# Kernel tuning notes

Measured on AMD Instinct MI355X. Metric: run time of the kernel, lower is better.

Reference implementation:

```python
import math
import jax, jax.numpy as jnp
import numpy as np

L, D, H, F, V, S = 4, 1024, 16, 4096, 50257, 2048
HS = D // H
EPS = 1e-5
STD = 0.02


def setup_inputs() -> dict:
    key = jax.random.key(0)
    keys = iter(jax.random.split(key, 24))

    def rn(shape):
        return (jax.random.normal(next(keys), shape, jnp.float32) * STD)

    inp = {
        "input_ids": jax.random.randint(next(keys), (1, S), 0, V, dtype=jnp.int64),
        "tok_emb": rn((V, D)),
        "pos_emb": rn((S, D)),
        # per-layer stacked params; linear weights stored [in, out]
        "Wq": rn((L, D, D)), "bq": jnp.zeros((L, D)),
        "Wk": rn((L, D, D)), "bk": jnp.zeros((L, D)),
        "Wv": rn((L, D, D)), "bv": jnp.zeros((L, D)),
        "Wo": rn((L, D, D)), "bo": jnp.zeros((L, D)),
        "W1": rn((L, D, F)), "b1": jnp.zeros((L, F)),
        "W2": rn((L, F, D)), "b2": jnp.zeros((L, D)),
        "ln1w": jnp.ones((L, D)), "ln1b": jnp.zeros((L, D)),
        "ln2w": jnp.ones((L, D)), "ln2b": jnp.zeros((L, D)),
        "lnfw": jnp.ones((D,)), "lnfb": jnp.zeros((D,)),
        "lm_head": rn((V, D)),  # torch Linear weight layout [out, in]
    }
    return inp


def _layernorm(x, w, b):
    m = jnp.mean(x, axis=-1, keepdims=True)
    v = jnp.mean(jnp.square(x - m), axis=-1, keepdims=True)
    return (x - m) * jax.lax.rsqrt(v + EPS) * w + b


def reference(input_ids, tok_emb, pos_emb, Wq, bq, Wk, bk, Wv, bv, Wo, bo,
              W1, b1, W2, b2, ln1w, ln1b, ln2w, ln2b, lnfw, lnfb, lm_head):
    B, Sq = input_ids.shape
    h = tok_emb[input_ids] + pos_emb[None, :Sq]  # [B,S,D]
    causal = jnp.tril(jnp.ones((Sq, Sq), dtype=bool))
    scale = 1.0 / math.sqrt(HS)

    def block(h, p):
        wq, bq_, wk, bk_, wv, bv_, wo, bo_, w1, b1_, w2, b2_, l1w, l1b, l2w, l2b = p
        x = _layernorm(h, l1w, l1b)
        q = (x @ wq + bq_).reshape(B, Sq, H, HS).transpose(0, 2, 1, 3)
        k = (x @ wk + bk_).reshape(B, Sq, H, HS).transpose(0, 2, 1, 3)
        v = (x @ wv + bv_).reshape(B, Sq, H, HS).transpose(0, 2, 1, 3)
        scores = jnp.einsum('bhqd,bhkd->bhqk', q, k) * scale
        scores = jnp.where(causal, scores, jnp.finfo(scores.dtype).min)
        attn = jax.nn.softmax(scores, axis=-1)  # dropout is identity at eval
        out = jnp.einsum('bhqk,bhkd->bhqd', attn, v)
        out = out.transpose(0, 2, 1, 3).reshape(B, Sq, D)
        h = h + out @ wo + bo_
        x = _layernorm(h, l2w, l2b)
        h = h + jax.nn.gelu(x @ w1 + b1_, approximate=False) @ w2 + b2_
        return h, None

    h, _ = jax.lax.scan(block, h, (Wq, bq, Wk, bk, Wv, bv, Wo, bo,
                                   W1, b1, W2, b2, ln1w, ln1b, ln2w, ln2b))
    h = _layernorm(h, lnfw, lnfb)
    logits = h @ lm_head.T  # [B,S,V]
    return logits
```

## Files before the change

### kernel.cpp

```cpp
#include <hip/hip_runtime.h>
#include <math.h>
#include <stdint.h>


#define SEQ 2048
#define DIM 1024
#define NHEAD 16
#define FFN 4096
#define VOCAB 50257
#define NLAYER 4
#define LNEPS 1e-5f
#define QKVD 3072
#define KVB 128

using bf16x8 = __attribute__((ext_vector_type(8))) short;
using s16x4  = __attribute__((ext_vector_type(4))) short;
using f32x4  = __attribute__((ext_vector_type(4))) float;
using fl4    = __attribute__((ext_vector_type(4))) float;

static __device__ __forceinline__ short f2bf(float f) {
  uint32_t u = __float_as_uint(f);
  u = (u + 0x7fffu + ((u >> 16) & 1u)) >> 16;
  return (short)u;
}
static __device__ __forceinline__ float bf2f(short s) {
  return __uint_as_float(((uint32_t)(uint16_t)s) << 16);
}
static __device__ __forceinline__ void gload_lds16(const void* g, void* l) {
  __builtin_amdgcn_global_load_lds((const __attribute__((address_space(1))) void*)g,
                                   (__attribute__((address_space(3))) void*)l, 16, 0, 0);
}

__global__ void embed_kernel(const int* __restrict__ ids,
                             const float* __restrict__ tok,
                             const float* __restrict__ pos,
                             float* __restrict__ h) {
  int i = blockIdx.x * blockDim.x + threadIdx.x;
  if (i < SEQ * DIM) {
    int s = i / DIM, d = i % DIM;
    h[i] = tok[(long)ids[s] * DIM + d] + pos[i];
  }
}

__global__ void ln_kernel(const float* __restrict__ x, const float* __restrict__ w,
                          const float* __restrict__ b, short* __restrict__ y) {
  int row = blockIdx.x;
  const float* xr = x + (long)row * DIM;
  short* yr = y + (long)row * DIM;
  int tid = threadIdx.x;
  float v0 = xr[tid], v1 = xr[tid + 256], v2 = xr[tid + 512], v3 = xr[tid + 768];
  __shared__ float red[8];
  float s = v0 + v1 + v2 + v3;
#pragma unroll
  for (int o = 32; o >= 1; o >>= 1) s += __shfl_xor(s, o);
  if ((tid & 63) == 0) red[tid >> 6] = s;
  __syncthreads();
  float mean = (red[0] + red[1] + red[2] + red[3]) * (1.f / DIM);
  float d0 = v0 - mean, d1 = v1 - mean, d2 = v2 - mean, d3 = v3 - mean;
  float q = d0 * d0 + d1 * d1 + d2 * d2 + d3 * d3;
#pragma unroll
  for (int o = 32; o >= 1; o >>= 1) q += __shfl_xor(q, o);
  if ((tid & 63) == 0) red[4 + (tid >> 6)] = q;
  __syncthreads();
  float var = (red[4] + red[5] + red[6] + red[7]) * (1.f / DIM);
  float rstd = rsqrtf(var + LNEPS);
  yr[tid]       = f2bf(d0 * rstd * w[tid] + b[tid]);
  yr[tid + 256] = f2bf(d1 * rstd * w[tid + 256] + b[tid + 256]);
  yr[tid + 512] = f2bf(d2 * rstd * w[tid + 512] + b[tid + 512]);
  yr[tid + 768] = f2bf(d3 * rstd * w[tid + 768] + b[tid + 768]);
}

__global__ void reduce_ln(const float* __restrict__ part, const float* __restrict__ bias,
                          const float* __restrict__ lnw, const float* __restrict__ lnb,
                          float* __restrict__ h, short* __restrict__ x) {
  const long MN = (long)SEQ * DIM;
  int row = blockIdx.x, tid = threadIdx.x;
  long off = (long)row * DIM + tid * 4;
  fl4 hv = *(const fl4*)(h + off);
  fl4 p0 = *(const fl4*)(part + off);
  fl4 p1 = *(const fl4*)(part + MN + off);
  fl4 bv = *(const fl4*)(bias + tid * 4);
  float v[4];
#pragma unroll
  for (int u = 0; u < 4; u++) v[u] = hv[u] + p0[u] + p1[u] + bv[u];
  __shared__ float red[8];
  float s = v[0] + v[1] + v[2] + v[3];
#pragma unroll
  for (int o = 32; o >= 1; o >>= 1) s += __shfl_xor(s, o);
  if ((tid & 63) == 0) red[tid >> 6] = s;
  __syncthreads();
  float mean = (red[0] + red[1] + red[2] + red[3]) * (1.f / DIM);
  float d[4], q = 0.f;
#pragma unroll
  for (int u = 0; u < 4; u++) { d[u] = v[u] - mean; q += d[u] * d[u]; }
#pragma unroll
  for (int o = 32; o >= 1; o >>= 1) q += __shfl_xor(q, o);
  if ((tid & 63) == 0) red[4 + (tid >> 6)] = q;
  fl4 hw; hw[0] = v[0]; hw[1] = v[1]; hw[2] = v[2]; hw[3] = v[3];
  *(fl4*)(h + off) = hw;
  __syncthreads();
  float var = (red[4] + red[5] + red[6] + red[7]) * (1.f / DIM);
  float rstd = rsqrtf(var + LNEPS);
  fl4 w = *(const fl4*)(lnw + tid * 4);
  fl4 bb = *(const fl4*)(lnb + tid * 4);
  s16x4 o;
#pragma unroll
  for (int u = 0; u < 4; u++) o[u] = f2bf(d[u] * rstd * w[u] + bb[u]);
  *(s16x4*)(x + off) = o;
}

struct Prep {
  const float *wq, *wk, *wv, *wo, *w1, *w2, *bq, *bk, *bv;
  short *qkvT, *woT, *w1T, *w2T;
  float* bias3;
};
__global__ void prep_kernel(Prep p) {
  int t = blockIdx.x;
  if (t >= 3072) {
    for (int k = threadIdx.x; k < QKVD; k += 256)
      p.bias3[k] = k < DIM ? p.bq[k] : (k < 2 * DIM ? p.bk[k - DIM] : p.bv[k - 2 * DIM]);
    return;
  }
  const float* in; short* out; int Kd, Nd, r0, c0;
  if (t < 1024) {
    int m = t >> 8, lt = t & 255;
    const float* srcs[4] = {p.wq, p.wk, p.wv, p.wo};
    short* dsts[4] = {p.qkvT, p.qkvT + (long)DIM * DIM, p.qkvT + (long)2 * DIM * DIM, p.woT};
    in = srcs[m]; out = dsts[m]; Kd = DIM; Nd = DIM;
    c0 = (lt & 15) * 64; r0 = (lt >> 4) * 64;
  } else if (t < 2048) {
    int lt = t - 1024; in = p.w1; out = p.w1T; Kd = DIM; Nd = FFN;
    c0 = (lt & 63) * 64; r0 = (lt >> 6) * 64;
  } else {
    int lt = t - 2048; in = p.w2; out = p.w2T; Kd = FFN; Nd = DIM;
    c0 = (lt & 15) * 64; r0 = (lt >> 4) * 64;
  }
  __shared__ float ts[64][65];
  int tid = threadIdx.x;
  int lr = tid >> 4, lc4 = (tid & 15) * 4;
#pragma unroll
  for (int i = 0; i < 4; i++) {
    fl4 v = *(const fl4*)(in + (long)(r0 + lr + i * 16) * Nd + c0 + lc4);
    ts[lr + i * 16][lc4] = v[0]; ts[lr + i * 16][lc4 + 1] = v[1];
    ts[lr + i * 16][lc4 + 2] = v[2]; ts[lr + i * 16][lc4 + 3] = v[3];
  }
  __syncthreads();
#pragma unroll
  for (int i = 0; i < 2; i++) {
    int oc = (tid >> 3) + i * 32, seg = tid & 7;
    bf16x8 o;
#pragma unroll
    for (int u = 0; u < 8; u++) o[u] = f2bf(ts[seg * 8 + u][oc]);
    *(bf16x8*)(out + (long)(c0 + oc) * Kd + r0 + seg * 8) = o;
  }
}

__global__ void transpose_v(const short* __restrict__ qkv, short* __restrict__ vt) {
  __shared__ short t[64][72];
  int s0 = blockIdx.x * 64, c0 = blockIdx.y * 64;
  int tid = threadIdx.x;
#pragma unroll
  for (int i = 0; i < 2; i++) {
    int ca = i * 256 + tid;
    int row = ca >> 3, cp = ca & 7;
    bf16x8 v = *(const bf16x8*)(qkv + (long)(s0 + row) * QKVD + 2 * DIM + c0 + cp * 8);
    *(bf16x8*)&t[row][cp * 8] = v;
  }
  __syncthreads();
#pragma unroll
  for (int i = 0; i < 2; i++) {
    int ca = i * 256 + tid;
    int crow = ca >> 3, sp = ca & 7;
    bf16x8 o;
#pragma unroll
    for (int u = 0; u < 8; u++) o[u] = t[sp * 8 + u][crow];
    *(bf16x8*)(vt + (long)(c0 + crow) * SEQ + s0 + sp * 8) = o;
  }
}

__global__ void conv_bf16(const float* __restrict__ in, short* __restrict__ out, long n4) {
  long i = (long)blockIdx.x * blockDim.x + threadIdx.x;
  long stride = (long)gridDim.x * blockDim.x;
  for (; i < n4; i += stride) {
    fl4 v = *(const fl4*)(in + i * 4);
    s16x4 o;
    o[0] = f2bf(v[0]); o[1] = f2bf(v[1]); o[2] = f2bf(v[2]); o[3] = f2bf(v[3]);
    *(s16x4*)(out + i * 4) = o;
  }
}

template <bool GELU, bool BIAS, bool OUTBF16, int KS, bool XCDSWZ>
__global__ __launch_bounds__(256, 4) void gemm_small(
    const short* __restrict__ A, const short* __restrict__ Bt,
    const float* __restrict__ bias, void* __restrict__ Cout, int N, int Kfull) {
  __shared__ short lds[3][(64 + 128) * 32];
  const int tid = threadIdx.x, wid = tid >> 6, lane = tid & 63;
  const int l16 = lane & 15, lg = lane >> 4;
  int bx = blockIdx.x, by = blockIdx.y;
  if (XCDSWZ) {
    int gx = gridDim.x, nwg = gx * gridDim.y;
    int flat = by * gx + bx;
    int nf = (flat & 7) * (nwg >> 3) + (flat >> 3);
    bx = nf % gx; by = nf / gx;
  }
  const long m0 = (long)bx * 64, n0 = (long)by * 128;
  const int K = Kfull / KS;
  const int kbase = blockIdx.z * K;
  const int NT = K / 32;
  const int wm = wid >> 1, wn = wid & 1;

#define STG(t, b)                                                               \
  {                                                                             \
    short* As_ = lds[b];                                                        \
    short* Bs_ = lds[b] + 64 * 32;                                              \
    int kk_ = kbase + (t) * 32;                                                 \
    {                                                                           \
      int row_ = tid >> 2, cp_ = tid & 3, c_ = cp_ ^ ((row_ >> 1) & 3);         \
      gload_lds16(A + (m0 + row_) * (long)Kfull + kk_ + c_ * 8,                 \
                  As_ + (wid * 64) * 8);                                        \
    }                                                                           \
    _Pragma("unroll")                                                           \
    for (int i_ = 0; i_ < 2; i_++) {                                            \
      int ca_ = i_ * 256 + tid;                                                 \
      int row_ = ca_ >> 2, cp_ = ca_ & 3, c_ = cp_ ^ ((row_ >> 1) & 3);         \
      gload_lds16(Bt + (long)(n0 + row_) * Kfull + kk_ + c_ * 8,                \
                  Bs_ + (i_ * 256 + wid * 64) * 8);                             \
    }                                                                           \
  }

  f32x4 acc[2][4] = {};
  STG(0, 0);
  STG(1, 1);
  asm volatile("s_waitcnt vmcnt(3)" ::: "memory");
  __builtin_amdgcn_s_barrier();
  __builtin_amdgcn_sched_barrier(0);

  for (int t = 0; t < NT; t++) {
    const int b = t % 3;
    if (t + 2 < NT) STG(t + 2, (t + 2) % 3);
    const short* As = lds[b];
    const short* Bs = lds[b] + 64 * 32;
    bf16x8 af[2], bfr[4];
#pragma unroll
    for (int m = 0; m < 2; m++) {
      int row = wm * 32 + m * 16 + l16;
      af[m] = *(const bf16x8*)((const char*)As + row * 64 + ((lg ^ ((row >> 1) & 3)) * 16));
    }
#pragma unroll
    for (int n = 0; n < 4; n++) {
      int row = wn * 64 + n * 16 + l16;
      bfr[n] = *(const bf16x8*)((const char*)Bs + row * 64 + ((lg ^ ((row >> 1) & 3)) * 16));
    }
    __builtin_amdgcn_s_setprio(1);
#pragma unroll
    for (int m = 0; m < 2; m++)
#pragma unroll
      for (int n = 0; n < 4; n++)
        acc[m][n] = __builtin_amdgcn_mfma_f32_16x16x32_bf16(af[m], bfr[n], acc[m][n], 0, 0, 0);
    __builtin_amdgcn_s_setprio(0);
    if (t + 2 < NT) {
      asm volatile("s_waitcnt vmcnt(3)" ::: "memory");
    } else if (t + 1 < NT) {
      asm volatile("s_waitcnt vmcnt(0)" ::: "memory");
    }
    if (t + 1 < NT) {
      __builtin_amdgcn_s_barrier();
      __builtin_amdgcn_sched_barrier(0);
    }
  }
#undef STG

  const int lr4 = lg * 4;
  if (KS == 1) {
#pragma unroll
    for (int m = 0; m < 2; m++)
#pragma unroll
      for (int n = 0; n < 4; n++)
#pragma unroll
        for (int r = 0; r < 4; r++) {
          long row = m0 + wm * 32 + m * 16 + lr4 + r;
          long col = n0 + wn * 64 + n * 16 + l16;
          float v = acc[m][n][r];
          if (BIAS) v += bias[col];
          if (GELU) v = 0.5f * v * (1.f + erff(v * 0.70710678118f));
          if (OUTBF16) ((short*)Cout)[row * (long)N + col] = f2bf(v);
          else ((float*)Cout)[row * (long)N + col] = v;
        }
  } else {
    long M = (long)gridDim.x * 64;
    float* P = (float*)Cout + (long)blockIdx.z * M * N;
#pragma unroll
    for (int m = 0; m < 2; m++)
#pragma unroll
      for (int n = 0; n < 4; n++)
#pragma unroll
        for (int r = 0; r < 4; r++) {
          long row = m0 + wm * 32 + m * 16 + lr4 + r;
          long col = n0 + wn * 64 + n * 16 + l16;
          P[row * (long)N + col] = acc[m][n][r];
        }
  }
}

template <bool GELU, bool BIAS, bool OUTBF16, bool XCDSWZ>
__global__ __launch_bounds__(256, 3) void gemm4(
    const short* __restrict__ A, const short* __restrict__ Bt,
    const float* __restrict__ bias, void* __restrict__ Cout, int N, int Kfull) {
  __shared__ short lds[3][(128 + 128) * 32];
  const int tid = threadIdx.x, wid = tid >> 6, lane = tid & 63;
  const int l16 = lane & 15, lg = lane >> 4;
  int bx = blockIdx.x, by = blockIdx.y;
  if (XCDSWZ) {
    int gx = gridDim.x, nwg = gx * gridDim.y;
    int flat = by * gx + bx;
    int nf = (flat & 7) * (nwg >> 3) + (flat >> 3);
    bx = nf % gx; by = nf / gx;
  }
  const long m0 = (long)bx * 128, n0 = (long)by * 128;
  const int NT = Kfull / 32;
  const int wr = (wid >> 1) * 64, wc = (wid & 1) * 64;

#define STAGE4(t, b)                                                            \
  {                                                                             \
    short* As_ = lds[b];                                                        \
    short* Bs_ = lds[b] + 128 * 32;                                             \
    int kk_ = (t) * 32;                                                         \
    _Pragma("unroll")                                                           \
    for (int i_ = 0; i_ < 2; i_++) {                                            \
      int ca_ = i_ * 256 + tid;                                                 \
      int row_ = ca_ >> 2, cp_ = ca_ & 3, c_ = cp_ ^ ((row_ >> 1) & 3);         \
      gload_lds16(A + (m0 + row_) * (long)Kfull + kk_ + c_ * 8,                 \
                  As_ + (i_ * 256 + wid * 64) * 8);                             \
    }                                                                           \
    _Pragma("unroll")                                                           \
    for (int i_ = 0; i_ < 2; i_++) {                                            \
      int ca_ = i_ * 256 + tid;                                                 \
      int row_ = ca_ >> 2, cp_ = ca_ & 3, c_ = cp_ ^ ((row_ >> 1) & 3);         \
      gload_lds16(Bt + (long)(n0 + row_) * Kfull + kk_ + c_ * 8,                \
                  Bs_ + (i_ * 256 + wid * 64) * 8);                             \
    }                                                                           \
  }

  f32x4 acc[4][4] = {};
  STAGE4(0, 0);
  STAGE4(1, 1);
  asm volatile("s_waitcnt vmcnt(4)" ::: "memory");
  __builtin_amdgcn_s_barrier();
  __builtin_amdgcn_sched_barrier(0);

  for (int t = 0; t < NT; t++) {
    const int b = t % 3;
    if (t + 2 < NT) STAGE4(t + 2, (t + 2) % 3);
    const short* As = lds[b];
    const short* Bs = lds[b] + 128 * 32;
    bf16x8 af[4], bfr[4];
#pragma unroll
    for (int m = 0; m < 4; m++) {
      int row = wr + m * 16 + l16;
      af[m] = *(const bf16x8*)((const char*)As + row * 64 + ((lg ^ ((row >> 1) & 3)) * 16));
    }
#pragma unroll
    for (int n = 0; n < 4; n++) {
      int row = wc + n * 16 + l16;
      bfr[n] = *(const bf16x8*)((const char*)Bs + row * 64 + ((lg ^ ((row >> 1) & 3)) * 16));
    }
    __builtin_amdgcn_s_setprio(1);
#pragma unroll
    for (int m = 0; m < 4; m++)
#pragma unroll
      for (int n = 0; n < 4; n++)
        acc[m][n] = __builtin_amdgcn_mfma_f32_16x16x32_bf16(af[m], bfr[n], acc[m][n], 0, 0, 0);
    __builtin_amdgcn_s_setprio(0);
    if (t + 2 < NT) {
      asm volatile("s_waitcnt vmcnt(4)" ::: "memory");
    } else if (t + 1 < NT) {
      asm volatile("s_waitcnt vmcnt(0)" ::: "memory");
    }
    if (t + 1 < NT) {
      __builtin_amdgcn_s_barrier();
      __builtin_amdgcn_sched_barrier(0);
    }
  }
#undef STAGE4

  const int lr4 = lg * 4;
#pragma unroll
  for (int m = 0; m < 4; m++)
#pragma unroll
    for (int n = 0; n < 4; n++)
#pragma unroll
      for (int r = 0; r < 4; r++) {
        long row = m0 + wr + m * 16 + lr4 + r;
        long col = n0 + wc + n * 16 + l16;
        float v = acc[m][n][r];
        if (BIAS) v += bias[col];
        if (GELU) v = 0.5f * v * (1.f + erff(v * 0.70710678118f));
        if (OUTBF16) ((short*)Cout)[row * (long)N + col] = f2bf(v);
        else ((float*)Cout)[row * (long)N + col] = v;
      }
}

__global__ __launch_bounds__(512, 1) void gemm256p(
    const short* __restrict__ A, const short* __restrict__ Bt,
    float* __restrict__ C, int N, int K, int totTiles) {
  __shared__ short ldsA[2][256 * 64];
  __shared__ short ldsB[2][256 * 64];
  const int tid = threadIdx.x, wid = tid >> 6, lane = tid & 63;
  const int l16 = lane & 15, lg = lane >> 4;
  const int wm = wid >> 2, wn = wid & 3;
  const int bid = blockIdx.x, nb = gridDim.x;
  const int ntiles = (totTiles - bid + nb - 1) / nb;
  const int TOT = ntiles * 16;

  auto tileMN = [&](int ord, long& m0, long& n0) {
    int j = bid + ord * nb;
    m0 = (long)(j & 7) * 256;
    n0 = (long)(j >> 3) * 256;
  };
  auto SA = [&](int s, int r0) {
    long m0s, n0s; tileMN(s >> 4, m0s, n0s);
    int row = r0 + wid * 8 + (lane >> 3);
    int c = (lane & 7) ^ (row & 7);
    gload_lds16(A + (m0s + row) * (long)K + (s & 15) * 64 + c * 8,
                &ldsA[s & 1][(r0 + wid * 8) * 64]);
  };
  auto SB = [&](int s, int r0) {
    long m0s, n0s; tileMN(s >> 4, m0s, n0s);
    int row = r0 + wid * 8 + (lane >> 3);
    int c = (lane & 7) ^ (row & 7);
    int rowb = (int)n0s + row;
    if (rowb > N - 1) rowb = N - 1;
    gload_lds16(Bt + (long)rowb * K + (s & 15) * 64 + c * 8,
                &ldsB[s & 1][(r0 + wid * 8) * 64]);
  };

  f32x4 acc[8][4] = {};
  bf16x8 bfr[4][2];

  auto PH = [&](int b, int q) {
    bf16x8 af[2][2];
    if (q == 0) {
#pragma unroll
      for (int nf = 0; nf < 4; nf++) {
        int row = wn * 64 + nf * 16 + l16;
#pragma unroll
        for (int ks = 0; ks < 2; ks++)
          bfr[nf][ks] = *(const bf16x8*)((const char*)&ldsB[b][0] + row * 128 +
                                         (((ks * 4 + lg) ^ (row & 7)) * 16));
      }
    }
#pragma unroll
    for (int j = 0; j < 2; j++) {
      int row = wm * 128 + (q * 2 + j) * 16 + l16;
#pragma unroll
      for (int ks = 0; ks < 2; ks++)
        af[j][ks] = *(const bf16x8*)((const char*)&ldsA[b][0] + row * 128 +
                                     (((ks * 4 + lg) ^ (row & 7)) * 16));
    }
    __builtin_amdgcn_s_barrier();
    __builtin_amdgcn_s_setprio(1);
#pragma unroll
    for (int ks = 0; ks < 2; ks++)
#pragma unroll
      for (int j = 0; j < 2; j++)
#pragma unroll
        for (int nf = 0; nf < 4; nf++)
          acc[q * 2 + j][nf] =
              __builtin_amdgcn_mfma_f32_16x16x32_bf16(af[j][ks], bfr[nf][ks],
                                                      acc[q * 2 + j][nf], 0, 0, 0);
    __builtin_amdgcn_s_setprio(0);
  };

  SA(0, 0); SA(0, 64); SA(0, 128); SA(0, 192);
  SB(0, 0); SB(0, 64); SB(0, 128); SB(0, 192);
  SA(1, 0); SA(1, 128);
  asm volatile("s_waitcnt vmcnt(2)" ::: "memory");
  __builtin_amdgcn_s_barrier();

  for (int it = 0; it < TOT / 2; it++) {
    const int e = 2 * it, o = e + 1;
    const bool more = (e + 2) < TOT;
    SA(o, 64); SA(o, 192);
    PH(0, 0);
    __builtin_amdgcn_s_barrier();
    SB(o, 0); SB(o, 64);
    PH(0, 1);
    __builtin_amdgcn_s_barrier();
    SB(o, 128); SB(o, 192);
    PH(0, 2);
    __builtin_amdgcn_s_barrier();
    if (more) { SA(e + 2, 0); SA(e + 2, 128); }
    PH(0, 3);
    if (more) asm volatile("s_waitcnt vmcnt(2)" ::: "memory");
    else      asm volatile("s_waitcnt vmcnt(0)" ::: "memory");
    __builtin_amdgcn_s_barrier();
    if (more) { SA(e + 2, 64); SA(e + 2, 192); }
    PH(1, 0);
    __builtin_amdgcn_s_barrier();
    if (more) { SB(e + 2, 0); SB(e + 2, 64); }
    PH(1, 1);
    __builtin_amdgcn_s_barrier();
    if (more) { SB(e + 2, 128); SB(e + 2, 192); }
    PH(1, 2);
    __builtin_amdgcn_s_barrier();
    if (more) { SA(e + 3, 0); SA(e + 3, 128); }
    PH(1, 3);
    if (more) {
      asm volatile("s_waitcnt vmcnt(2)" ::: "memory");
      __builtin_amdgcn_s_barrier();
    } else {
      asm volatile("s_waitcnt vmcnt(0)" ::: "memory");
    }
    if ((o & 15) == 15) {
      long m0c, n0c; tileMN(o >> 4, m0c, n0c);
#pragma unroll
      for (int mf = 0; mf < 8; mf++)
#pragma unroll
        for (int nf = 0; nf < 4; nf++)
#pragma unroll
          for (int r = 0; r < 4; r++) {
            long row = m0c + wm * 128 + mf * 16 + lg * 4 + r;
            long col = n0c + wn * 64 + nf * 16 + l16;
            if (col < N) C[row * (long)N + col] = acc[mf][nf][r];
            acc[mf][nf][r] = 0.f;
          }
    }
  }
}

__global__ __launch_bounds__(256) void attn_mfma(const short* __restrict__ qkv,
                                                 const short* __restrict__ vtg,
                                                 short* __restrict__ Oa) {
  int hh = blockIdx.x, qb = blockIdx.y;
  int q0 = qb * 64;
  int tid = threadIdx.x, wv = tid >> 6, lane = tid & 63;
  int l16 = lane & 15, lg = lane >> 4;
  int hcol = hh * 64;
  __shared__ short Ks[2][KVB * 64];
  __shared__ short Vt[2][64 * KVB];
  __shared__ short Pl[4][16 * KVB];

  bf16x8 qf[2];
  {
    const short* qrow = qkv + (long)(q0 + wv * 16 + l16) * QKVD + hcol;
#pragma unroll
    for (int dc = 0; dc < 2; dc++) {
      bf16x8 t = *(const bf16x8*)(qrow + dc * 32 + lg * 8);
#pragma unroll
      for (int j = 0; j < 8; j++) t[j] = f2bf(bf2f(t[j]) * 0.125f);
      qf[dc] = t;
    }
  }
  f32x4 of[4] = {};
  float mrun[4], lrun[4];
#pragma unroll
  for (int r = 0; r < 4; r++) { mrun[r] = -3e38f; lrun[r] = 0.f; }

#define STAGEKV(kt_, b_)                                                        \
  {                                                                             \
    int k0_ = (kt_) * KVB;                                                      \
    _Pragma("unroll")                                                           \
    for (int i = 0; i < 4; i++) {                                               \
      int ca = i * 256 + tid;                                                   \
      int row = ca >> 3, cp = ca & 7, c = cp ^ (row & 7);                       \
      gload_lds16(qkv + (long)(k0_ + row) * QKVD + DIM + hcol + c * 8,          \
                  (short*)Ks[b_] + (i * 256 + wv * 64) * 8);                    \
    }                                                                           \
    _Pragma("unroll")                                                           \
    for (int i = 0; i < 4; i++) {                                               \
      int ca = i * 256 + tid;                                                   \
      int row = ca >> 4, cp = ca & 15, c = cp ^ (row & 7);                      \
      gload_lds16(vtg + (long)(hcol + row) * SEQ + k0_ + c * 8,                 \
                  (short*)Vt[b_] + (i * 256 + wv * 64) * 8);                    \
    }                                                                           \
  }

  int nt = qb / 2 + 1;
  STAGEKV(0, 0);
  asm volatile("s_waitcnt vmcnt(0)" ::: "memory");
  __builtin_amdgcn_s_barrier();

  for (int kt = 0; kt < nt; kt++) {
    const int cur = kt & 1;
    if (kt + 1 < nt) STAGEKV(kt + 1, cur ^ 1);
    int k0 = kt * KVB;

    f32x4 sacc[8] = {};
    __builtin_amdgcn_s_setprio(1);
#pragma unroll
    for (int kc = 0; kc < 8; kc++) {
      int row = kc * 16 + l16;
#pragma unroll
      for (int dc = 0; dc < 2; dc++) {
        bf16x8 kf = *(const bf16x8*)((const char*)Ks[cur] + row * 128 + (((dc * 4 + lg) ^ (row & 7)) * 16));
        sacc[kc] = __builtin_amdgcn_mfma_f32_16x16x32_bf16(qf[dc], kf, sacc[kc], 0, 0, 0);
      }
    }
    __builtin_amdgcn_s_setprio(0);

    float sv[8][4], pf[8][4];
#pragma unroll
    for (int kc = 0; kc < 8; kc++)
#pragma unroll
      for (int r = 0; r < 4; r++) sv[kc][r] = sacc[kc][r];
    if (kt == nt - 1) {
#pragma unroll
      for (int kc = 0; kc < 8; kc++)
#pragma unroll
        for (int r = 0; r < 4; r++) {
          int kg = k0 + kc * 16 + l16;
          int rg = q0 + wv * 16 + lg * 4 + r;
          if (kg > rg) sv[kc][r] = -3e38f;
        }
    }
    float corr[4];
#pragma unroll
    for (int r = 0; r < 4; r++) {
      float m01 = fmaxf(sv[0][r], sv[1][r]), m23 = fmaxf(sv[2][r], sv[3][r]);
      float m45 = fmaxf(sv[4][r], sv[5][r]), m67 = fmaxf(sv[6][r], sv[7][r]);
      float mt = fmaxf(fmaxf(m01, m23), fmaxf(m45, m67));
#pragma unroll
      for (int o = 8; o >= 1; o >>= 1) mt = fmaxf(mt, __shfl_xor(mt, o));
      float mn = fmaxf(mrun[r], mt);
      corr[r] = __expf(mrun[r] - mn);
      mrun[r] = mn;
      float ps = 0.f;
#pragma unroll
      for (int kc = 0; kc < 8; kc++) {
        float p = __expf(sv[kc][r] - mn);
        pf[kc][r] = p;
        ps += p;
      }
#pragma unroll
      for (int o = 8; o >= 1; o >>= 1) ps += __shfl_xor(ps, o);
      lrun[r] = lrun[r] * corr[r] + ps;
    }
#pragma unroll
    for (int c = 0; c < 4; c++)
#pragma unroll
      for (int r = 0; r < 4; r++) of[c][r] *= corr[r];
#pragma unroll
    for (int kc = 0; kc < 8; kc++)
#pragma unroll
      for (int r = 0; r < 4; r++) {
        int row = lg * 4 + r, col = kc * 16 + l16;
        int chunk = col >> 3;
        *(short*)((char*)Pl[wv] + row * 256 + ((chunk ^ (row & 7)) * 16) + (col & 7) * 2) = f2bf(pf[kc][r]);
      }
    bf16x8 pfr[4];
#pragma unroll
    for (int kc2 = 0; kc2 < 4; kc2++) {
      int cl = kc2 * 4 + lg;
      pfr[kc2] = *(const bf16x8*)((const char*)Pl[wv] + l16 * 256 + ((cl ^ (l16 & 7)) * 16));
    }
    __builtin_amdgcn_s_setprio(1);
#pragma unroll
    for (int c = 0; c < 4; c++)
#pragma unroll
      for (int kc2 = 0; kc2 < 4; kc2++) {
        int vrow = c * 16 + l16;
        int cl = kc2 * 4 + lg;
        bf16x8 vf = *(const bf16x8*)((const char*)Vt[cur] + vrow * 256 + ((cl ^ (vrow & 7)) * 16));
        of[c] = __builtin_amdgcn_mfma_f32_16x16x32_bf16(pfr[kc2], vf, of[c], 0, 0, 0);
      }
    __builtin_amdgcn_s_setprio(0);
    if (kt + 1 < nt) {
      asm volatile("s_waitcnt vmcnt(0)" ::: "memory");
      __builtin_amdgcn_s_barrier();
      __builtin_amdgcn_sched_barrier(0);
    }
  }
#undef STAGEKV
#pragma unroll
  for (int c = 0; c < 4; c++)
#pragma unroll
    for (int r = 0; r < 4; r++) {
      int rowg = q0 + wv * 16 + lg * 4 + r;
      int colg = hcol + c * 16 + l16;
      Oa[(long)rowg * DIM + colg] = f2bf(of[c][r] / lrun[r]);
    }
}

extern "C" void kernel_launch(void* const* d_in, const int* in_sizes, int n_in,
                              void* d_out, int out_size, void* d_ws, size_t ws_size,
                              hipStream_t stream) {
  const int* ids = (const int*)d_in[0];
  const float* tok = (const float*)d_in[1];
  const float* pos = (const float*)d_in[2];
  const float* Wq = (const float*)d_in[3];
  const float* bq = (const float*)d_in[4];
  const float* Wk = (const float*)d_in[5];
  const float* bk = (const float*)d_in[6];
  const float* Wv = (const float*)d_in[7];
  const float* bv = (const float*)d_in[8];
  const float* Wo = (const float*)d_in[9];
  const float* bo = (const float*)d_in[10];
  const float* W1 = (const float*)d_in[11];
  const float* b1 = (const float*)d_in[12];
  const float* W2 = (const float*)d_in[13];
  const float* b2 = (const float*)d_in[14];
  const float* ln1w = (const float*)d_in[15];
  const float* ln1b = (const float*)d_in[16];
  const float* ln2w = (const float*)d_in[17];
  const float* ln2b = (const float*)d_in[18];
  const float* lnfw = (const float*)d_in[19];
  const float* lnfb = (const float*)d_in[20];
  const float* lmh = (const float*)d_in[21];
  float* out = (float*)d_out;

  char* wsb = (char*)d_ws;
  float* h = (float*)wsb;
  short* x = (short*)(wsb + 8388608);
  char* big = wsb + 8388608 + 4194304;
  short* qkv  = (short*)big;
  short* a    = (short*)(big + 12582912);
  short* vt   = (short*)(big + 16777216);
  short* fbuf = (short*)(big + 20971520);
  float* pproj = (float*)fbuf;
  float* pffn2 = (float*)big;
  char* wdyn = big + 37748736;
  short* wqkvT = (short*)wdyn;
  short* woT   = (short*)(wdyn + 6291456);
  short* w1T   = (short*)(wdyn + 8388608);
  short* w2T   = (short*)(wdyn + 16777216);
  float* bias3 = (float*)(wdyn + 25165824);
  short* lmhB = (short*)big;

  embed_kernel<<<(SEQ * DIM + 255) / 256, 256, 0, stream>>>(ids, tok, pos, h);
  ln_kernel<<<SEQ, 256, 0, stream>>>(h, ln1w, ln1b, x);

  dim3 gQKV(SEQ / 64, QKVD / 128);
  dim3 gPROJ(SEQ / 64, DIM / 128, 2);
  dim3 gFFN1(SEQ / 128, FFN / 128);
  dim3 gFFN2(SEQ / 64, DIM / 128, 2);

  for (int l = 0; l < NLAYER; l++) {
    Prep p;
    p.wq = Wq + (long)l * DIM * DIM; p.wk = Wk + (long)l * DIM * DIM;
    p.wv = Wv + (long)l * DIM * DIM; p.wo = Wo + (long)l * DIM * DIM;
    p.w1 = W1 + (long)l * DIM * FFN; p.w2 = W2 + (long)l * FFN * DIM;
    p.bq = bq + (long)l * DIM; p.bk = bk + (long)l * DIM; p.bv = bv + (long)l * DIM;
    p.qkvT = wqkvT; p.woT = woT; p.w1T = w1T; p.w2T = w2T; p.bias3 = bias3;
    prep_kernel<<<3073, 256, 0, stream>>>(p);

    gemm_small<false, true, true, 1, true><<<gQKV, 256, 0, stream>>>(x, wqkvT, bias3, qkv, QKVD, DIM);
    transpose_v<<<dim3(SEQ / 64, DIM / 64), 256, 0, stream>>>(qkv, vt);
    attn_mfma<<<dim3(NHEAD, SEQ / 64), 256, 0, stream>>>(qkv, vt, a);
    gemm_small<false, false, false, 2, true><<<gPROJ, 256, 0, stream>>>(a, woT, nullptr, pproj, DIM, DIM);
    reduce_ln<<<SEQ, 256, 0, stream>>>(pproj, bo + (long)l * DIM,
                                       ln2w + (long)l * DIM, ln2b + (long)l * DIM, h, x);
    gemm4<true, true, true, true><<<gFFN1, 256, 0, stream>>>(x, w1T, b1 + (long)l * FFN, fbuf, FFN, DIM);
    gemm_small<false, false, false, 2, true><<<gFFN2, 256, 0, stream>>>(fbuf, w2T, nullptr, pffn2, DIM, FFN);
    const float* nw = (l < NLAYER - 1) ? ln1w + (long)(l + 1) * DIM : lnfw;
    const float* nb = (l < NLAYER - 1) ? ln1b + (long)(l + 1) * DIM : lnfb;
    reduce_ln<<<SEQ, 256, 0, stream>>>(pffn2, b2 + (long)l * DIM, nw, nb, h, x);
  }

  conv_bf16<<<2048, 256, 0, stream>>>(lmh, lmhB, (long)VOCAB * DIM / 4);
  gemm256p<<<dim3(256), 512, 0, stream>>>(x, lmhB, out, VOCAB, DIM,
                                          (SEQ / 256) * ((VOCAB + 255) / 256));
}
```

Before: 1.118 ms.

## Remap LM-head GEMM tiles per XCD and simplify double-buffer pipeline schedule

The persistent 256x256 LM-head GEMM now assigns tiles so that consecutive block IDs (round-robined across the 8 XCDs) get neighbouring tiles. This is meant to improve L2 reuse of the shared B (lm_head) rows within each XCD, and it assumes a grid of 256 blocks. The K-loop is rewritten from a two-stage unrolled schedule to a single-stage loop. B is now prefetched before A for the next K-step, with adjusted vmcnt waits. This reduces code size and changes how loads overlap with MFMA phases, but it may expose more load latency.

```diff
diff --git a/kernel.cpp b/kernel.cpp
--- a/kernel.cpp
+++ b/kernel.cpp
@@ -408,14 +408,15 @@
   const int tid = threadIdx.x, wid = tid >> 6, lane = tid & 63;
   const int l16 = lane & 15, lg = lane >> 4;
   const int wm = wid >> 2, wn = wid & 3;
-  const int bid = blockIdx.x, nb = gridDim.x;
-  const int ntiles = (totTiles - bid + nb - 1) / nb;
-  const int TOT = ntiles * 16;
+  const int bid = blockIdx.x;
+  const int f0 = (bid & 7) * 32 + (bid >> 3);
+  const int nt = (totTiles - f0 + 255) / 256;
+  const int TOT = nt * 16;
 
   auto tileMN = [&](int ord, long& m0, long& n0) {
-    int j = bid + ord * nb;
-    m0 = (long)(j & 7) * 256;
-    n0 = (long)(j >> 3) * 256;
+    int f = f0 + (ord << 8);
+    m0 = (long)(f & 7) * 256;
+    n0 = (long)(f >> 3) * 256;
   };
   auto SA = [&](int s, int r0) {
     long m0s, n0s; tileMN(s >> 4, m0s, n0s);
@@ -471,48 +472,32 @@
     __builtin_amdgcn_s_setprio(0);
   };
 
-  SA(0, 0); SA(0, 64); SA(0, 128); SA(0, 192);
   SB(0, 0); SB(0, 64); SB(0, 128); SB(0, 192);
-  SA(1, 0); SA(1, 128);
+  SA(0, 0); SA(0, 128); SA(0, 64); SA(0, 192);
   asm volatile("s_waitcnt vmcnt(2)" ::: "memory");
   __builtin_amdgcn_s_barrier();
 
-  for (int it = 0; it < TOT / 2; it++) {
-    const int e = 2 * it, o = e + 1;
-    const bool more = (e + 2) < TOT;
-    SA(o, 64); SA(o, 192);
-    PH(0, 0);
+  for (int s = 0; s < TOT; s++) {
+    const int b = s & 1;
+    const bool stg = (s + 1) < TOT;
+    if (stg) { SB(s + 1, 0); SB(s + 1, 64); }
+    PH(b, 0);
     __builtin_amdgcn_s_barrier();
-    SB(o, 0); SB(o, 64);
-    PH(0, 1);
+    if (stg) { SB(s + 1, 128); SB(s + 1, 192); }
+    PH(b, 1);
+    if (stg) asm volatile("s_waitcnt vmcnt(4)" ::: "memory");
+    else     asm volatile("s_waitcnt vmcnt(0)" ::: "memory");
     __builtin_amdgcn_s_barrier();
-    SB(o, 128); SB(o, 192);
-    PH(0, 2);
+    if (stg) { SA(s + 1, 0); SA(s + 1, 128); }
+    PH(b, 2);
     __builtin_amdgcn_s_barrier();
-    if (more) { SA(e + 2, 0); SA(e + 2, 128); }
-    PH(0, 3);
-    if (more) asm volatile("s_waitcnt vmcnt(2)" ::: "memory");
-    else      asm volatile("s_waitcnt vmcnt(0)" ::: "memory");
+    if (stg) { SA(s + 1, 64); SA(s + 1, 192); }
+    PH(b, 3);
+    if (stg) asm volatile("s_waitcnt vmcnt(2)" ::: "memory");
+    else     asm volatile("s_waitcnt vmcnt(0)" ::: "memory");
     __builtin_amdgcn_s_barrier();
-    if (more) { SA(e + 2, 64); SA(e + 2, 192); }
-    PH(1, 0);
-    __builtin_amdgcn_s_barrier();
-    if (more) { SB(e + 2, 0); SB(e + 2, 64); }
-    PH(1, 1);
-    __builtin_amdgcn_s_barrier();
-    if (more) { SB(e + 2, 128); SB(e + 2, 192); }
-    PH(1, 2);
-    __builtin_amdgcn_s_barrier();
-    if (more) { SA(e + 3, 0); SA(e + 3, 128); }
-    PH(1, 3);
-    if (more) {
-      asm volatile("s_waitcnt vmcnt(2)" ::: "memory");
-      __builtin_amdgcn_s_barrier();
-    } else {
-      asm volatile("s_waitcnt vmcnt(0)" ::: "memory");
-    }
-    if ((o & 15) == 15) {
-      long m0c, n0c; tileMN(o >> 4, m0c, n0c);
+    if ((s & 15) == 15) {
+      long m0c, n0c; tileMN(s >> 4, m0c, n0c);
 #pragma unroll
       for (int mf = 0; mf < 8; mf++)
 #pragma unroll
```

Result: slower. 1.152 ms (+3.0%).
